# Kernel tuning notes

Measured on AMD Instinct MI355X. Metric: run time of the kernel, lower is better.

## Reference

```python
import jax, jax.numpy as jnp
import numpy as np
import math

B, T, C, NH, LEVEL = 2, 2048, 1024, 16, 3


def _build_sets(T, level):
    # hierarchical dyadic sets: levels `level`..floor(log2(T)), step 2^l
    sets = []
    levelmax = int(math.floor(math.log2(T)))
    for l in range(level, levelmax + 1):
        step = 2 ** l
        for i in range(T // step):
            sets.append((i * step, (i + 1) * step - 1))
    b = np.asarray(sets, dtype=np.int32)
    return b[:, 0], b[:, 1]


def setup_inputs() -> dict:
    key = jax.random.key(0)
    kx, kw1, kw2 = jax.random.split(key, 3)
    x = jax.random.normal(kx, (B, T, C), dtype=jnp.float32)
    # torch nn.Linear stores weight as (out_features, in_features); y = x @ W.T
    W_attn = jax.random.normal(kw1, (3 * C, C), dtype=jnp.float32) * (C ** -0.5)
    W_proj = jax.random.normal(kw2, (C, C), dtype=jnp.float32) * (C ** -0.5)
    return {"x": x, "W_attn": W_attn, "W_proj": W_proj}


def _get_slice(xc, l_idx, r_idx):
    # xc: (B,NH,T,hs) cumulative sums; returns sum over [l_idx, r_idx]
    r = xc[:, :, r_idx, :]
    l = xc[:, :, l_idx - 1, :] * (l_idx >= 1)[None, None, :, None].astype(xc.dtype)
    return r - l


def _forward(x, W_attn, W_proj):
    hs = C // NH
    scale = hs ** -0.5
    qkv = x @ W_attn.T                      # (B,T,3C)
    q, k, v = jnp.split(qkv, 3, axis=2)
    heads = lambda t: t.reshape(B, T, NH, hs).transpose(0, 2, 1, 3)  # (B,NH,T,hs)
    q, k, v = heads(q), heads(k), heads(v)
    phi = lambda t: jax.nn.elu(t) + 1.0     # feature_map = 'elu_plus'
    q_phi, k_phi = phi(q), phi(k)
    k_cum = jnp.cumsum(k_phi, axis=2)
    v_cum = jnp.cumsum(v, axis=2)

    l_np, r_np = _build_sets(T, LEVEL)
    l_idx, r_idx = jnp.asarray(l_np), jnp.asarray(r_np)
    K = _get_slice(k_cum, l_idx, r_idx)     # (B,NH,S,hs)
    V = _get_slice(v_cum, l_idx, r_idx)

    t_idx = jnp.arange(T)
    mask = t_idx[:, None] >= r_idx[None, :]                 # (T,S)
    logits = jnp.einsum('bhtd,bhsd->bhts', q, K) * scale    # raw q here (as in source)
    logits = jnp.where(mask[None, None], logits, -jnp.inf)

    # tail term over last (t mod 2^level)+1 tokens, uses q_phi
    Lmin = 2 ** LEVEL
    tail_len = t_idx % Lmin + 1
    l_tail = t_idx - tail_len + 1
    K_tail = _get_slice(k_cum, l_tail, t_idx)               # (B,NH,T,hs)
    V_tail = _get_slice(v_cum, l_tail, t_idx)
    tail_logit = jnp.sum(q_phi * K_tail, axis=-1) * scale   # (B,NH,T)

    full = jnp.concatenate([logits, tail_logit[..., None]], axis=-1)
    att = jax.nn.softmax(full, axis=-1)
    out = jnp.einsum('bhts,bhsd->bhtd', att[..., :-1], V) + att[..., -1:] * V_tail
    out = out.transpose(0, 2, 1, 3).reshape(B, T, C)
    return out @ W_proj.T


def reference(x, W_attn, W_proj):
    return _forward(x, W_attn, W_proj)
```

## Files before the change

kernel.cpp:

```cpp
#include <hip/hip_runtime.h>
#include <hip/hip_bf16.h>
#include <stdint.h>

#define B_    2
#define T_    2048
#define CD    1024
#define NH_   16
#define HS_   64
#define NSETS 511
#define NSP   512
#define QKV_LD 3072
#define NEGBIG (-3.4e38f)

typedef __attribute__((ext_vector_type(8))) short  short8;
typedef __attribute__((ext_vector_type(4))) float  f32x4;
typedef _Float16 half8v __attribute__((ext_vector_type(8)));

__device__ __forceinline__ unsigned short f2bf(float f) {
  unsigned u = __float_as_uint(f);
  unsigned r = 0x7FFFu + ((u >> 16) & 1u);
  return (unsigned short)((u + r) >> 16);
}
__device__ __forceinline__ float bf2f(unsigned short h) {
  return __uint_as_float(((unsigned)h) << 16);
}
__device__ __forceinline__ unsigned short f2h(float v) {
  _Float16 h = (_Float16)v;
  return __builtin_bit_cast(unsigned short, h);
}
__device__ __forceinline__ float elu1(float x) {
  return x > 0.f ? x + 1.f : __expf(x);
}
__device__ __forceinline__ void gload16(const unsigned short* g, short* l) {
  __builtin_amdgcn_global_load_lds(
      (const __attribute__((address_space(1))) unsigned int*)g,
      (__attribute__((address_space(3))) unsigned int*)l, 16, 0, 0);
}

__global__ __launch_bounds__(256) void split3_kernel(
    const float* __restrict__ x, const float* __restrict__ Wa,
    const float* __restrict__ Wp,
    unsigned short* __restrict__ xh, unsigned short* __restrict__ xl,
    unsigned short* __restrict__ xf,
    unsigned short* __restrict__ waqh, unsigned short* __restrict__ waql,
    unsigned short* __restrict__ wakvf, unsigned short* __restrict__ wph) {
  int bid = blockIdx.x;
  int t = threadIdx.x;
  if (bid < 16384) {
    int i = bid * 256 + t;
    float v = x[i];
    unsigned short h = f2bf(v);
    xh[i] = h;
    xl[i] = f2bf(v - bf2f(h));
    xf[i] = f2h(v);
  } else if (bid < 20480) {
    int i = (bid - 16384) * 256 + t;
    float v = Wa[i];
    unsigned short h = f2bf(v);
    waqh[i] = h;
    waql[i] = f2bf(v - bf2f(h));
  } else if (bid < 28672) {
    int i = (bid - 20480) * 256 + t;
    wakvf[i] = f2h(Wa[1048576 + i]);
  } else {
    int i = (bid - 28672) * 256 + t;
    wph[i] = f2bf(Wp[i]);
  }
}

template<int SPLIT, int BN, int F16>
__device__ __forceinline__ void gemm_body(
    short* lds,
    const unsigned short* __restrict__ Ah, const unsigned short* __restrict__ Al,
    const unsigned short* __restrict__ Bh, const unsigned short* __restrict__ Bl,
    float* __restrict__ Cmat, int K, int ldc, int row0, int col0)
{
  constexpr int NB   = BN / 16;
  constexpr int ALD  = 8 * (1 + SPLIT);
  constexpr int TL   = ALD + NB * (1 + SPLIT);
  constexpr int PW   = TL / 4;
  constexpr int ASH  = (1 + SPLIT) * 4096;
  constexpr int ABYT = ASH * 2;
  constexpr int NC   = BN / 32;

  const int tid  = threadIdx.x;
  const int lane = tid & 63;
  const int w    = tid >> 6;
  const int wr   = w >> 1, wc = w & 1;

  f32x4 acc[4][NC];
  #pragma unroll
  for (int a = 0; a < 4; ++a)
    #pragma unroll
    for (int b = 0; b < NC; ++b)
      acc[a][b] = (f32x4){0.f, 0.f, 0.f, 0.f};

  const int rlane = lane & 15;
  const int kgrp  = lane >> 4;
  const int rsw   = (kgrp ^ (rlane & 3) ^ ((rlane >> 2) & 3)) << 4;

  const int slr = lane >> 2;
  const int sch = (lane & 3) ^ (slr & 3) ^ ((slr >> 2) & 3);

  for (int kt = 0; kt < K; kt += 32) {
    __syncthreads();
    #pragma unroll
    for (int li = 0; li < PW; ++li) {
      int L = w * PW + li;
      const unsigned short* src; int dsts; size_t rowb;
      if (L < 8)                { src = Ah; rowb = (size_t)row0 + L * 16;       dsts = L * 512; }
      else if (SPLIT && L < 16) { src = Al; rowb = (size_t)row0 + (L - 8) * 16; dsts = 4096 + (L - 8) * 512; }
      else {
        int Lb = L - ALD;
        if (!SPLIT || Lb < NB) { src = Bh; rowb = (size_t)col0 + Lb * 16;        dsts = ASH + Lb * 512; }
        else                   { src = Bl; rowb = (size_t)col0 + (Lb - NB) * 16; dsts = ASH + BN * 32 + (Lb - NB) * 512; }
      }
      gload16(src + (rowb + slr) * K + kt + (sch << 3), lds + dsts + lane * 8);
    }
    __syncthreads();

    short8 aH[4], bH[NC], aL[4], bL[NC];
    #pragma unroll
    for (int m = 0; m < 4; ++m) {
      int r = wr * 64 + m * 16 + rlane;
      aH[m] = *(const short8*)((const char*)lds + r * 64 + rsw);
      if (SPLIT) aL[m] = *(const short8*)((const char*)lds + 8192 + r * 64 + rsw);
    }
    #pragma unroll
    for (int n = 0; n < NC; ++n) {
      int c = wc * (BN / 2) + n * 16 + rlane;
      bH[n] = *(const short8*)((const char*)lds + ABYT + c * 64 + rsw);
      if (SPLIT) bL[n] = *(const short8*)((const char*)lds + ABYT + BN * 64 + c * 64 + rsw);
    }
    #pragma unroll
    for (int mm = 0; mm < 4; ++mm)
      #pragma unroll
      for (int nn = 0; nn < NC; ++nn) {
        if (F16) {
          acc[mm][nn] = __builtin_amdgcn_mfma_f32_16x16x32_f16(
              __builtin_bit_cast(half8v, aH[mm]), __builtin_bit_cast(half8v, bH[nn]),
              acc[mm][nn], 0, 0, 0);
        } else {
          acc[mm][nn] = __builtin_amdgcn_mfma_f32_16x16x32_bf16(aH[mm], bH[nn], acc[mm][nn], 0, 0, 0);
          if (SPLIT) {
            acc[mm][nn] = __builtin_amdgcn_mfma_f32_16x16x32_bf16(aH[mm], bL[nn], acc[mm][nn], 0, 0, 0);
            acc[mm][nn] = __builtin_amdgcn_mfma_f32_16x16x32_bf16(aL[mm], bH[nn], acc[mm][nn], 0, 0, 0);
          }
        }
      }
  }

  const int rl = (lane >> 4) * 4;
  const int cl = lane & 15;
  #pragma unroll
  for (int mm = 0; mm < 4; ++mm)
    #pragma unroll
    for (int nn = 0; nn < NC; ++nn)
      #pragma unroll
      for (int r = 0; r < 4; ++r) {
        int row = row0 + wr * 64 + mm * 16 + rl + r;
        int col = col0 + wc * (BN / 2) + nn * 16 + cl;
        Cmat[(size_t)row * ldc + col] = acc[mm][nn][r];
      }
}

template<int SPLIT, int BN, int F16>
__global__ __launch_bounds__(256) void gemm_bt(
    const unsigned short* __restrict__ Ah, const unsigned short* __restrict__ Al,
    const unsigned short* __restrict__ Bh, const unsigned short* __restrict__ Bl,
    float* __restrict__ Cmat, int M, int N, int K, int ldc)
{
  __shared__ short lds[(1 + SPLIT) * 4096 + (1 + SPLIT) * BN * 32];
  const int nwg = gridDim.x;
  const int cpx = nwg >> 3;
  const int bid = blockIdx.x;
  const int swb = (bid & 7) * cpx + (bid >> 3);
  const int nbx = N / BN;
  const int bx = swb % nbx;
  const int by = swb / nbx;
  gemm_body<SPLIT, BN, F16>(lds, Ah, Al, Bh, Bl, Cmat, K, ldc, by * 128, bx * BN);
}

__global__ __launch_bounds__(256) void cs_part(const float* __restrict__ qkv,
                                               float* __restrict__ part) {
  int blk = blockIdx.x;
  int q   = blk & 1;
  int seg = (blk >> 1) & 63;
  int b   = blk >> 7;
  int c   = threadIdx.x * 4;
  const float* src = qkv + (size_t)(b * T_ + seg * 32) * QKV_LD + CD + q * CD + c;
  float4 s = {0.f, 0.f, 0.f, 0.f};
  #pragma unroll 4
  for (int j = 0; j < 32; ++j) {
    float4 v = *(const float4*)(src + (size_t)j * QKV_LD);
    if (q == 0) {
      s.x += elu1(v.x); s.y += elu1(v.y); s.z += elu1(v.z); s.w += elu1(v.w);
    } else {
      s.x += v.x; s.y += v.y; s.z += v.z; s.w += v.w;
    }
  }
  *(float4*)(part + ((size_t)(b * 64 + seg) * 2048) + q * 1024 + c) = s;
}

__global__ __launch_bounds__(256) void cs_final(const float* __restrict__ qkv,
                                                const float* __restrict__ part,
                                                float* __restrict__ kcum,
                                                float* __restrict__ vcum) {
  int blk = blockIdx.x;
  int q   = blk & 1;
  int seg = (blk >> 1) & 63;
  int b   = blk >> 7;
  int c   = threadIdx.x * 4;
  int h   = c >> 6, d = c & 63;
  float4 s = {0.f, 0.f, 0.f, 0.f};
  const float* pb = part + (size_t)(b * 64) * 2048 + q * 1024 + c;
  #pragma unroll 8
  for (int ss = 0; ss < seg; ++ss) {
    float4 p = *(const float4*)(pb + (size_t)ss * 2048);
    s.x += p.x; s.y += p.y; s.z += p.z; s.w += p.w;
  }
  const float* src = qkv + (size_t)(b * T_ + seg * 32) * QKV_LD + CD + q * CD + c;
  float* dst = (q == 0 ? kcum : vcum) + ((size_t)(b * NH_ + h) * T_ + seg * 32) * HS_ + d;
  #pragma unroll 4
  for (int j = 0; j < 32; ++j) {
    float4 v = *(const float4*)(src + (size_t)j * QKV_LD);
    if (q == 0) {
      s.x += elu1(v.x); s.y += elu1(v.y); s.z += elu1(v.z); s.w += elu1(v.w);
    } else {
      s.x += v.x; s.y += v.y; s.z += v.z; s.w += v.w;
    }
    *(float4*)(dst + (size_t)j * HS_) = s;
  }
}

__global__ __launch_bounds__(256) void build_sets2(
    const float* __restrict__ kcum, const float* __restrict__ vcum,
    unsigned short* __restrict__ Ksh, unsigned short* __restrict__ Ksl,
    unsigned short* __restrict__ Vst, int* __restrict__ r_srt)
{
  __shared__ int   lr[64], lli[64];
  __shared__ float vt[64][65];
  const int bh = blockIdx.x >> 3;
  const int s0 = (blockIdx.x & 7) * 64;
  const int tid = threadIdx.x;

  for (int s = tid; s < NSP; s += 256) {
    int r, li, rank;
    if (s == NSETS) { r = 0x7fffffff; li = 0; rank = NSETS; }
    else {
      int lvl = 3, base = 0;
      while (s >= base + (T_ >> lvl)) { base += T_ >> lvl; ++lvl; }
      int i = s - base;
      int m = (i + 1) << lvl;
      r = m - 1; li = i << lvl;
      rank = lvl - 3;
      #pragma unroll
      for (int j = 3; j <= 11; ++j) rank += (m - 8) >> j;
    }
    if (rank >= s0 && rank < s0 + 64) {
      lr[rank - s0]  = r;
      lli[rank - s0] = li;
      if (bh == 0) r_srt[rank] = r;
    }
  }
  __syncthreads();

  const int sl = tid >> 2;
  const int dq = (tid & 3) * 16;
  const int r  = lr[sl], li = lli[sl];
  const size_t orow = ((size_t)(bh << 9) + s0 + sl) * HS_ + dq;
  short8 kh0, kh1, kl0, kl1;
  if (r == 0x7fffffff) {
    #pragma unroll
    for (int j = 0; j < 8; ++j) { kh0[j]=0; kh1[j]=0; kl0[j]=0; kl1[j]=0; }
    #pragma unroll
    for (int j = 0; j < 16; ++j) vt[sl][dq + j] = 0.f;
  } else {
    const float* kr0 = kcum + ((size_t)bh * T_ + r) * HS_ + dq;
    const float* vr0 = vcum + ((size_t)bh * T_ + r) * HS_ + dq;
    const float* kr1 = kcum + ((size_t)bh * T_ + (li - 1)) * HS_ + dq;
    const float* vr1 = vcum + ((size_t)bh * T_ + (li - 1)) * HS_ + dq;
    #pragma unroll
    for (int g = 0; g < 4; ++g) {
      float4 kv = *(const float4*)(kr0 + g * 4);
      float4 vv = *(const float4*)(vr0 + g * 4);
      if (li > 0) {
        float4 k1 = *(const float4*)(kr1 + g * 4);
        float4 v1 = *(const float4*)(vr1 + g * 4);
        kv.x -= k1.x; kv.y -= k1.y; kv.z -= k1.z; kv.w -= k1.w;
        vv.x -= v1.x; vv.y -= v1.y; vv.z -= v1.z; vv.w -= v1.w;
      }
      float ka[4] = {kv.x, kv.y, kv.z, kv.w};
      float va[4] = {vv.x, vv.y, vv.z, vv.w};
      #pragma unroll
      for (int j = 0; j < 4; ++j) {
        int e = g * 4 + j;
        unsigned short h = f2bf(ka[j]);
        unsigned short l = f2bf(ka[j] - bf2f(h));
        if (e < 8) { kh0[e] = (short)h; kl0[e] = (short)l; }
        else       { kh1[e - 8] = (short)h; kl1[e - 8] = (short)l; }
        vt[sl][dq + e] = va[j];
      }
    }
  }
  *(short8*)(Ksh + orow)     = kh0;
  *(short8*)(Ksh + orow + 8) = kh1;
  *(short8*)(Ksl + orow)     = kl0;
  *(short8*)(Ksl + orow + 8) = kl1;
  __syncthreads();

  const int d  = tid >> 2;
  const int sq = (tid & 3) * 16;
  short8 a, b2;
  #pragma unroll
  for (int j = 0; j < 8; ++j) {
    a[j]  = (short)f2bf(vt[sq + j][d]);
    b2[j] = (short)f2bf(vt[sq + 8 + j][d]);
  }
  unsigned short* dst = Vst + ((size_t)(bh << 6) + d) * NSP + s0 + sq;
  *(short8*)dst = a;
  *(short8*)(dst + 8) = b2;
}

__global__ __launch_bounds__(256) void attn_mfma(
    const float* __restrict__ qkv, const float* __restrict__ kcum,
    const float* __restrict__ vcum,
    const unsigned short* __restrict__ Ksh, const unsigned short* __restrict__ Ksl,
    const unsigned short* __restrict__ Vst, const int* __restrict__ r_srt,
    unsigned short* __restrict__ attnb)
{
  __shared__ short Pl[4 * 1024];
  __shared__ short KV[3 * 4096];
  __shared__ int   rs_lds[NSP];

  const int blk = blockIdx.x;
  const int xcd = blk & 7;
  const int j   = blk >> 3;
  const int bh  = xcd * 4 + (j >> 5);
  const int tch = (j + ((j >> 5) << 3)) & 31;
  const int b = bh >> 4, h = bh & 15;
  const int t0 = tch * 64;
  const int tid = threadIdx.x;
  const int lane = tid & 63;
  const int w = tid >> 6;
  const int col = lane & 15;
  const int kgrp = (lane >> 4) * 8;
  const float scale = 0.125f;

  const int srow = lane >> 3;
  const int scsw = ((lane & 7) ^ srow) * 8;

  auto stage_tile = [&](int s0) {
    #pragma unroll
    for (int L = w * 6; L < w * 6 + 6; ++L) {
      int a = L >> 3, i = L & 7;
      const unsigned short* src;
      if (a == 0)      src = Ksh + ((size_t)(bh << 9) + s0 + i * 8 + srow) * 64 + scsw;
      else if (a == 1) src = Ksl + ((size_t)(bh << 9) + s0 + i * 8 + srow) * 64 + scsw;
      else             src = Vst + ((size_t)(bh << 6) + i * 8 + srow) * NSP + s0 + scsw;
      gload16(src, KV + a * 4096 + i * 512 + lane * 8);
    }
  };

  short8 qh[2], ql[2];
  {
    int qrow = t0 + w * 16 + col;
    const float* qr = qkv + (size_t)(b * T_ + qrow) * QKV_LD + h * HS_;
    #pragma unroll
    for (int ks = 0; ks < 2; ++ks) {
      float4 v0 = *(const float4*)(qr + kgrp + ks * 32);
      float4 v1 = *(const float4*)(qr + kgrp + ks * 32 + 4);
      float vv[8] = {v0.x, v0.y, v0.z, v0.w, v1.x, v1.y, v1.z, v1.w};
      #pragma unroll
      for (int jj = 0; jj < 8; ++jj) {
        unsigned short hi = f2bf(vv[jj]);
        qh[ks][jj] = (short)hi;
        ql[ks][jj] = (short)f2bf(vv[jj] - bf2f(hi));
      }
    }
  }
  for (int s = tid; s < NSP; s += 256) rs_lds[s] = r_srt[s];

  int rows[4];
  #pragma unroll
  for (int r = 0; r < 4; ++r) rows[r] = t0 + w * 16 + (lane >> 4) * 4 + r;

  f32x4 O[4];
  float mrun[4], lsum[4];
  #pragma unroll
  for (int f = 0; f < 4; ++f) {
    O[f] = (f32x4){0.f, 0.f, 0.f, 0.f};
    mrun[f] = NEGBIG; lsum[f] = 0.f;
  }

  int nmax = 0;
  #pragma unroll
  for (int jj = 3; jj <= 11; ++jj) nmax += (t0 + 64) >> jj;
  const int ntiles = (nmax + 63) >> 6;

  for (int tile = 0; tile < ntiles; ++tile) {
    const int s0 = tile * 64;
    stage_tile(s0);
    __syncthreads();

    const char* kc = (const char*)KV;
    f32x4 S[4];
    #pragma unroll
    for (int f = 0; f < 4; ++f) S[f] = (f32x4){0.f, 0.f, 0.f, 0.f};

    #pragma unroll
    for (int ks = 0; ks < 2; ++ks) {
      int chnk = (lane >> 4) + ks * 4;
      #pragma unroll
      for (int f = 0; f < 4; ++f) {
        int so = f * 16 + col;
        int kb = so * 128 + ((chnk ^ (so & 7)) << 4);
        short8 bHv = *(const short8*)(kc + kb);
        short8 bLv = *(const short8*)(kc + 8192 + kb);
        S[f] = __builtin_amdgcn_mfma_f32_16x16x32_bf16(qh[ks], bHv, S[f], 0, 0, 0);
        S[f] = __builtin_amdgcn_mfma_f32_16x16x32_bf16(qh[ks], bLv, S[f], 0, 0, 0);
        S[f] = __builtin_amdgcn_mfma_f32_16x16x32_bf16(ql[ks], bHv, S[f], 0, 0, 0);
      }
    }

    int rsv[4];
    #pragma unroll
    for (int f = 0; f < 4; ++f) rsv[f] = rs_lds[s0 + f * 16 + col];

    float zv[4][4];
    #pragma unroll
    for (int f = 0; f < 4; ++f)
      #pragma unroll
      for (int r = 0; r < 4; ++r)
        zv[f][r] = (rsv[f] > rows[r]) ? NEGBIG : S[f][r] * scale;

    float mx[4];
    #pragma unroll
    for (int r = 0; r < 4; ++r)
      mx[r] = fmaxf(fmaxf(zv[0][r], zv[1][r]), fmaxf(zv[2][r], zv[3][r]));
    int pred = (mx[0] <= mrun[0] + 8.f) & (mx[1] <= mrun[1] + 8.f) &
               (mx[2] <= mrun[2] + 8.f) & (mx[3] <= mrun[3] + 8.f);
    if (!__all(pred)) {
      #pragma unroll
      for (int r = 0; r < 4; ++r) {
        float mt = mx[r];
        mt = fmaxf(mt, __shfl_xor(mt, 1));
        mt = fmaxf(mt, __shfl_xor(mt, 2));
        mt = fmaxf(mt, __shfl_xor(mt, 4));
        mt = fmaxf(mt, __shfl_xor(mt, 8));
        float mv = fmaxf(mrun[r], mt);
        float fs = __expf(mrun[r] - mv);
        lsum[r] *= fs;
        #pragma unroll
        for (int f = 0; f < 4; ++f) O[f][r] *= fs;
        mrun[r] = mv;
      }
    }

    char* pw = (char*)Pl + w * 2048;
    #pragma unroll
    for (int r = 0; r < 4; ++r) {
      int rowr = (lane >> 4) * 4 + r;
      int rswz = (rowr & 7) << 4;
      #pragma unroll
      for (int f = 0; f < 4; ++f) {
        float p = __expf(zv[f][r] - mrun[r]);
        p = (rsv[f] > rows[r]) ? 0.f : p;
        lsum[r] += p;
        int addr = (rowr * 128 + (f * 16 + col) * 2) ^ rswz;
        *(unsigned short*)(pw + addr) = f2bf(p);
      }
    }

    #pragma unroll
    for (int ks = 0; ks < 2; ++ks) {
      int chnk = (lane >> 4) + ks * 4;
      int pbyte = (col * 128 + (kgrp + ks * 32) * 2) ^ ((col & 7) << 4);
      short8 pa = *(const short8*)(pw + pbyte);
      #pragma unroll
      for (int f = 0; f < 4; ++f) {
        int dr = f * 16 + col;
        short8 bv = *(const short8*)(kc + 16384 + dr * 128 + ((chnk ^ (dr & 7)) << 4));
        O[f] = __builtin_amdgcn_mfma_f32_16x16x32_bf16(pa, bv, O[f], 0, 0, 0);
      }
    }

    __syncthreads();
  }

  float lrun[4];
  #pragma unroll
  for (int r = 0; r < 4; ++r) {
    float l = lsum[r];
    l += __shfl_xor(l, 1);
    l += __shfl_xor(l, 2);
    l += __shfl_xor(l, 4);
    l += __shfl_xor(l, 8);
    lrun[r] = l;
  }

  float ztail;
  {
    int trow = lane >> 2;
    int t = t0 + w * 16 + trow;
    int d0 = (lane & 3) * 16;
    const float* qr = qkv + (size_t)(b * T_ + t) * QKV_LD + h * HS_ + d0;
    float qv[16];
    #pragma unroll
    for (int jj = 0; jj < 4; ++jj) {
      float4 v = *(const float4*)(qr + jj * 4);
      qv[jj*4+0] = v.x; qv[jj*4+1] = v.y; qv[jj*4+2] = v.z; qv[jj*4+3] = v.w;
    }
    int lt = t & ~7;
    const float* kc1 = kcum + ((size_t)bh * T_ + t) * HS_ + d0;
    float kt[16];
    if (lt > 0) {
      const float* kc0 = kcum + ((size_t)bh * T_ + (lt - 1)) * HS_ + d0;
      #pragma unroll
      for (int jj = 0; jj < 16; ++jj) kt[jj] = kc1[jj] - kc0[jj];
    } else {
      #pragma unroll
      for (int jj = 0; jj < 16; ++jj) kt[jj] = kc1[jj];
    }
    float z = 0.f;
    #pragma unroll
    for (int jj = 0; jj < 16; ++jj) {
      float qp = qv[jj] > 0.f ? qv[jj] + 1.f : __expf(qv[jj]);
      z += qp * kt[jj];
    }
    z += __shfl_xor(z, 1);
    z += __shfl_xor(z, 2);
    ztail = z * scale;
  }

  #pragma unroll
  for (int r = 0; r < 4; ++r) {
    float zt = __shfl(ztail, ((lane >> 4) * 4 + r) * 4);
    float mv = fmaxf(mrun[r], zt);
    float fs = __expf(mrun[r] - mv);
    float pwgt = __expf(zt - mv);
    lrun[r] = lrun[r] * fs + pwgt;
    int tr = rows[r];
    int ltr = tr & ~7;
    #pragma unroll
    for (int f = 0; f < 4; ++f) {
      int d = f * 16 + col;
      float v1 = vcum[((size_t)bh * T_ + tr) * HS_ + d];
      float vt = (ltr > 0) ? v1 - vcum[((size_t)bh * T_ + (ltr - 1)) * HS_ + d] : v1;
      O[f][r] = O[f][r] * fs + pwgt * vt;
    }
  }

  #pragma unroll
  for (int r = 0; r < 4; ++r) {
    float inv = 1.f / lrun[r];
    unsigned short* orow = attnb + (size_t)(b * T_ + rows[r]) * CD + h * HS_;
    #pragma unroll
    for (int f = 0; f < 4; ++f)
      orow[f * 16 + col] = f2bf(O[f][r] * inv);
  }
}

extern "C" void kernel_launch(void* const* d_in, const int* in_sizes, int n_in,
                              void* d_out, int out_size, void* d_ws, size_t ws_size,
                              hipStream_t stream) {
  const float* x  = (const float*)d_in[0];
  const float* Wa = (const float*)d_in[1];
  const float* Wp = (const float*)d_in[2];
  float* out = (float*)d_out;

  char* ws = (char*)d_ws;
  size_t off = 0;
  auto alloc = [&](size_t bytes) -> char* {
    char* p = ws + off;
    off += (bytes + 255) & ~(size_t)255;
    return p;
  };

  const int M = B_ * T_;
  float* qkv  = (float*)alloc((size_t)M * QKV_LD * 4);
  float* kcum = (float*)alloc((size_t)B_ * NH_ * T_ * HS_ * 4);
  float* vcum = (float*)alloc((size_t)B_ * NH_ * T_ * HS_ * 4);
  float* part = (float*)alloc((size_t)B_ * 64 * 2048 * 4);
  unsigned short* wph = (unsigned short*)alloc((size_t)CD * CD * 2);

  unsigned short* xf    = (unsigned short*)kcum;
  unsigned short* wakvf = (unsigned short*)vcum;

  char* regionA = alloc((size_t)16777216);
  unsigned short* xh = (unsigned short*)regionA;
  unsigned short* xl = (unsigned short*)(regionA + (size_t)M * CD * 2);
  const size_t SETS_ELEMS = (size_t)B_ * NH_ * NSP * HS_;
  unsigned short* Ksh = (unsigned short*)regionA;
  unsigned short* Ksl = Ksh + SETS_ELEMS;
  unsigned short* Vst = (unsigned short*)(regionA + 2 * SETS_ELEMS * 2);
  int*            r_srt = (int*)(regionA + 3 * SETS_ELEMS * 2);

  char* regionB = alloc((size_t)12582912);
  unsigned short* waqh = (unsigned short*)regionB;
  unsigned short* waql = (unsigned short*)(regionB + (size_t)CD * CD * 2);
  unsigned short* attnb = (unsigned short*)regionB;

  split3_kernel<<<dim3(32768), dim3(256), 0, stream>>>(
      x, Wa, Wp, xh, xl, xf, waqh, waql, wakvf, wph);

  gemm_bt<1, 64, 0><<<dim3(512), dim3(256), 0, stream>>>(
      xh, xl, waqh, waql, qkv, M, 1024, CD, QKV_LD);

  gemm_bt<0, 128, 1><<<dim3(512), dim3(256), 0, stream>>>(
      xf, (const unsigned short*)nullptr, wakvf, (const unsigned short*)nullptr,
      qkv + 1024, M, 2048, CD, QKV_LD);

  cs_part<<<dim3(B_ * 64 * 2), dim3(256), 0, stream>>>(qkv, part);
  cs_final<<<dim3(B_ * 64 * 2), dim3(256), 0, stream>>>(qkv, part, kcum, vcum);

  build_sets2<<<dim3(B_ * NH_ * 8), dim3(256), 0, stream>>>(
      kcum, vcum, Ksh, Ksl, Vst, r_srt);

  attn_mfma<<<dim3(1024), dim3(256), 0, stream>>>(
      qkv, kcum, vcum, Ksh, Ksl, Vst, r_srt, attnb);

  gemm_bt<0, 64, 0><<<dim3(512), dim3(256), 0, stream>>>(
      attnb, (const unsigned short*)nullptr, wph, (const unsigned short*)nullptr,
      out, M, 1024, CD, CD);
}
```

Baseline: 185.9 us.

## Prefetch attention tiles into registers, fold scale into exp2, double cumsum segments

In the attention kernel, the direct global-to-LDS tile loads are replaced by register prefetch: the next tile is loaded into registers while the current one is computed, and the registers are written to LDS at the top of the next iteration. The softmax scale and log2(e) are folded into q before the bf16 hi/lo split so the kernel can use exp2f, and the lazy-rescale threshold is adjusted to match the base-2 domain. The cumulative-sum kernels use 16-row segments instead of 32, which doubles the block count and the size of the partial buffer. These changes add register pressure and a longer serial prefix loop in cs_final, and folding the scale before the split slightly changes rounding.

Measured after the change: 204.6 us. +10.1%, slower.

```diff
diff --git a/kernel.cpp b/kernel.cpp
--- a/kernel.cpp
+++ b/kernel.cpp
@@ -11,6 +11,7 @@
 #define NSP   512
 #define QKV_LD 3072
 #define NEGBIG (-3.4e38f)
+#define QSC   (0.125f * 1.44269504088896f)
 
 typedef __attribute__((ext_vector_type(8))) short  short8;
 typedef __attribute__((ext_vector_type(4))) float  f32x4;
@@ -185,13 +186,13 @@
                                                float* __restrict__ part) {
   int blk = blockIdx.x;
   int q   = blk & 1;
-  int seg = (blk >> 1) & 63;
-  int b   = blk >> 7;
+  int seg = (blk >> 1) & 127;
+  int b   = blk >> 8;
   int c   = threadIdx.x * 4;
-  const float* src = qkv + (size_t)(b * T_ + seg * 32) * QKV_LD + CD + q * CD + c;
+  const float* src = qkv + (size_t)(b * T_ + seg * 16) * QKV_LD + CD + q * CD + c;
   float4 s = {0.f, 0.f, 0.f, 0.f};
   #pragma unroll 4
-  for (int j = 0; j < 32; ++j) {
+  for (int j = 0; j < 16; ++j) {
     float4 v = *(const float4*)(src + (size_t)j * QKV_LD);
     if (q == 0) {
       s.x += elu1(v.x); s.y += elu1(v.y); s.z += elu1(v.z); s.w += elu1(v.w);
@@ -199,7 +200,7 @@
       s.x += v.x; s.y += v.y; s.z += v.z; s.w += v.w;
     }
   }
-  *(float4*)(part + ((size_t)(b * 64 + seg) * 2048) + q * 1024 + c) = s;
+  *(float4*)(part + ((size_t)(b * 128 + seg) * 2048) + q * 1024 + c) = s;
 }
 
 __global__ __launch_bounds__(256) void cs_final(const float* __restrict__ qkv,
@@ -208,21 +209,21 @@
                                                 float* __restrict__ vcum) {
   int blk = blockIdx.x;
   int q   = blk & 1;
-  int seg = (blk >> 1) & 63;
-  int b   = blk >> 7;
+  int seg = (blk >> 1) & 127;
+  int b   = blk >> 8;
   int c   = threadIdx.x * 4;
   int h   = c >> 6, d = c & 63;
   float4 s = {0.f, 0.f, 0.f, 0.f};
-  const float* pb = part + (size_t)(b * 64) * 2048 + q * 1024 + c;
+  const float* pb = part + (size_t)(b * 128) * 2048 + q * 1024 + c;
   #pragma unroll 8
   for (int ss = 0; ss < seg; ++ss) {
     float4 p = *(const float4*)(pb + (size_t)ss * 2048);
     s.x += p.x; s.y += p.y; s.z += p.z; s.w += p.w;
   }
-  const float* src = qkv + (size_t)(b * T_ + seg * 32) * QKV_LD + CD + q * CD + c;
-  float* dst = (q == 0 ? kcum : vcum) + ((size_t)(b * NH_ + h) * T_ + seg * 32) * HS_ + d;
+  const float* src = qkv + (size_t)(b * T_ + seg * 16) * QKV_LD + CD + q * CD + c;
+  float* dst = (q == 0 ? kcum : vcum) + ((size_t)(b * NH_ + h) * T_ + seg * 16) * HS_ + d;
   #pragma unroll 4
-  for (int j = 0; j < 32; ++j) {
+  for (int j = 0; j < 16; ++j) {
     float4 v = *(const float4*)(src + (size_t)j * QKV_LD);
     if (q == 0) {
       s.x += elu1(v.x); s.y += elu1(v.y); s.z += elu1(v.z); s.w += elu1(v.w);
@@ -329,9 +330,9 @@
     const unsigned short* __restrict__ Vst, const int* __restrict__ r_srt,
     unsigned short* __restrict__ attnb)
 {
-  __shared__ short Pl[4 * 1024];
-  __shared__ short KV[3 * 4096];
-  __shared__ int   rs_lds[NSP];
+  __shared__ __align__(16) short Pl[4 * 1024];
+  __shared__ __align__(16) short KV[3 * 4096];
+  __shared__ int rs_lds[NSP];
 
   const int blk = blockIdx.x;
   const int xcd = blk & 7;
@@ -345,22 +346,30 @@
   const int w = tid >> 6;
   const int col = lane & 15;
   const int kgrp = (lane >> 4) * 8;
-  const float scale = 0.125f;
 
   const int srow = lane >> 3;
   const int scsw = ((lane & 7) ^ srow) * 8;
 
-  auto stage_tile = [&](int s0) {
-    #pragma unroll
-    for (int L = w * 6; L < w * 6 + 6; ++L) {
-      int a = L >> 3, i = L & 7;
-      const unsigned short* src;
-      if (a == 0)      src = Ksh + ((size_t)(bh << 9) + s0 + i * 8 + srow) * 64 + scsw;
-      else if (a == 1) src = Ksl + ((size_t)(bh << 9) + s0 + i * 8 + srow) * 64 + scsw;
-      else             src = Vst + ((size_t)(bh << 6) + i * 8 + srow) * NSP + s0 + scsw;
-      gload16(src, KV + a * 4096 + i * 512 + lane * 8);
-    }
-  };
+  int nmax = 0;
+  #pragma unroll
+  for (int jj = 3; jj <= 11; ++jj) nmax += (t0 + 64) >> jj;
+  const int ntiles = (nmax + 63) >> 6;
+
+  const unsigned short* srcp[6];
+  int dsts[6], adv[6];
+  #pragma unroll
+  for (int li = 0; li < 6; ++li) {
+    int L = w * 6 + li;
+    int a = L >> 3, i = L & 7;
+    if (a == 0)      srcp[li] = Ksh + ((size_t)(bh << 9) + i * 8 + srow) * 64 + scsw;
+    else if (a == 1) srcp[li] = Ksl + ((size_t)(bh << 9) + i * 8 + srow) * 64 + scsw;
+    else             srcp[li] = Vst + ((size_t)(bh << 6) + i * 8 + srow) * NSP + scsw;
+    dsts[li] = (a * 4096 + i * 512 + lane * 8) * 2;
+    adv[li]  = (a < 2) ? 4096 : 64;
+  }
+  float4 stg[6];
+  #pragma unroll
+  for (int li = 0; li < 6; ++li) stg[li] = *(const float4*)srcp[li];
 
   short8 qh[2], ql[2];
   {
@@ -373,9 +382,10 @@
       float vv[8] = {v0.x, v0.y, v0.z, v0.w, v1.x, v1.y, v1.z, v1.w};
       #pragma unroll
       for (int jj = 0; jj < 8; ++jj) {
-        unsigned short hi = f2bf(vv[jj]);
+        float sv = vv[jj] * QSC;
+        unsigned short hi = f2bf(sv);
         qh[ks][jj] = (short)hi;
-        ql[ks][jj] = (short)f2bf(vv[jj] - bf2f(hi));
+        ql[ks][jj] = (short)f2bf(sv - bf2f(hi));
       }
     }
   }
@@ -393,15 +403,20 @@
     mrun[f] = NEGBIG; lsum[f] = 0.f;
   }
 
-  int nmax = 0;
-  #pragma unroll
-  for (int jj = 3; jj <= 11; ++jj) nmax += (t0 + 64) >> jj;
-  const int ntiles = (nmax + 63) >> 6;
-
   for (int tile = 0; tile < ntiles; ++tile) {
     const int s0 = tile * 64;
-    stage_tile(s0);
+    #pragma unroll
+    for (int li = 0; li < 6; ++li)
+      *(float4*)((char*)KV + dsts[li]) = stg[li];
     __syncthreads();
+
+    if (tile + 1 < ntiles) {
+      #pragma unroll
+      for (int li = 0; li < 6; ++li) {
+        srcp[li] += adv[li];
+        stg[li] = *(const float4*)srcp[li];
+      }
+    }
 
     const char* kc = (const char*)KV;
     f32x4 S[4];
@@ -432,14 +447,14 @@
     for (int f = 0; f < 4; ++f)
       #pragma unroll
       for (int r = 0; r < 4; ++r)
-        zv[f][r] = (rsv[f] > rows[r]) ? NEGBIG : S[f][r] * scale;
+        zv[f][r] = (rsv[f] > rows[r]) ? NEGBIG : S[f][r];
 
     float mx[4];
     #pragma unroll
     for (int r = 0; r < 4; ++r)
       mx[r] = fmaxf(fmaxf(zv[0][r], zv[1][r]), fmaxf(zv[2][r], zv[3][r]));
-    int pred = (mx[0] <= mrun[0] + 8.f) & (mx[1] <= mrun[1] + 8.f) &
-               (mx[2] <= mrun[2] + 8.f) & (mx[3] <= mrun[3] + 8.f);
+    int pred = (mx[0] <= mrun[0] + 11.5f) & (mx[1] <= mrun[1] + 11.5f) &
+               (mx[2] <= mrun[2] + 11.5f) & (mx[3] <= mrun[3] + 11.5f);
     if (!__all(pred)) {
       #pragma unroll
       for (int r = 0; r < 4; ++r) {
@@ -449,7 +464,7 @@
         mt = fmaxf(mt, __shfl_xor(mt, 4));
         mt = fmaxf(mt, __shfl_xor(mt, 8));
         float mv = fmaxf(mrun[r], mt);
-        float fs = __expf(mrun[r] - mv);
+        float fs = exp2f(mrun[r] - mv);
         lsum[r] *= fs;
         #pragma unroll
         for (int f = 0; f < 4; ++f) O[f][r] *= fs;
@@ -464,7 +479,7 @@
       int rswz = (rowr & 7) << 4;
       #pragma unroll
       for (int f = 0; f < 4; ++f) {
-        float p = __expf(zv[f][r] - mrun[r]);
+        float p = exp2f(zv[f][r] - mrun[r]);
         p = (rsv[f] > rows[r]) ? 0.f : p;
         lsum[r] += p;
         int addr = (rowr * 128 + (f * 16 + col) * 2) ^ rswz;
@@ -530,15 +545,15 @@
     }
     z += __shfl_xor(z, 1);
     z += __shfl_xor(z, 2);
-    ztail = z * scale;
+    ztail = z * QSC;
   }
 
   #pragma unroll
   for (int r = 0; r < 4; ++r) {
     float zt = __shfl(ztail, ((lane >> 4) * 4 + r) * 4);
     float mv = fmaxf(mrun[r], zt);
-    float fs = __expf(mrun[r] - mv);
-    float pwgt = __expf(zt - mv);
+    float fs = exp2f(mrun[r] - mv);
+    float pwgt = exp2f(zt - mv);
     lrun[r] = lrun[r] * fs + pwgt;
     int tr = rows[r];
     int ltr = tr & ~7;
@@ -581,7 +596,7 @@
   float* qkv  = (float*)alloc((size_t)M * QKV_LD * 4);
   float* kcum = (float*)alloc((size_t)B_ * NH_ * T_ * HS_ * 4);
   float* vcum = (float*)alloc((size_t)B_ * NH_ * T_ * HS_ * 4);
-  float* part = (float*)alloc((size_t)B_ * 64 * 2048 * 4);
+  float* part = (float*)alloc((size_t)B_ * 128 * 2048 * 4);
   unsigned short* wph = (unsigned short*)alloc((size_t)CD * CD * 2);
 
   unsigned short* xf    = (unsigned short*)kcum;
@@ -611,8 +626,8 @@
       xf, (const unsigned short*)nullptr, wakvf, (const unsigned short*)nullptr,
       qkv + 1024, M, 2048, CD, QKV_LD);
 
-  cs_part<<<dim3(B_ * 64 * 2), dim3(256), 0, stream>>>(qkv, part);
-  cs_final<<<dim3(B_ * 64 * 2), dim3(256), 0, stream>>>(qkv, part, kcum, vcum);
+  cs_part<<<dim3(B_ * 128 * 2), dim3(256), 0, stream>>>(qkv, part);
+  cs_final<<<dim3(B_ * 128 * 2), dim3(256), 0, stream>>>(qkv, part, kcum, vcum);
 
   build_sets2<<<dim3(B_ * NH_ * 8), dim3(256), 0, stream>>>(
       kcum, vcum, Ksh, Ksl, Vst, r_srt);
```
